# Performance work log

Measured on AMD Instinct MI355X. Metric: run time of the kernel, lower is better.

## Reference

```python
import jax, jax.numpy as jnp
import numpy as np

N = 50000       # num nodes
E_DIR = 250000  # directed edges; doubled with inverses -> 500000
R = 100         # num relations; doubled -> 200
D = 32          # input/hidden dim
L = 6           # num layers
B = 4           # batch of queries
K = 33          # 1 positive + 32 negative tails
EPS = 1e-6


def setup_inputs() -> dict:
    key = jax.random.key(0)
    ks = jax.random.split(key, 12)
    src = jax.random.randint(ks[0], (E_DIR,), 0, N)
    dst = jax.random.randint(ks[1], (E_DIR,), 0, N)
    rel = jax.random.randint(ks[2], (E_DIR,), 0, R)
    # graph.undirected(add_inverse=True): append (t, h, r + R)
    edge_list = jnp.concatenate([
        jnp.stack([src, dst, rel], -1),
        jnp.stack([dst, src, rel + R], -1)], 0).astype(jnp.int32)
    h0 = jax.random.randint(ks[3], (B, 1), 0, N)
    h_index = jnp.tile(h0, (1, K)).astype(jnp.int32)   # constant per row (asserted by module)
    t_index = jax.random.randint(ks[4], (B, K), 0, N).astype(jnp.int32)
    r0 = jax.random.randint(ks[5], (B, 1), 0, R)
    r_index = jnp.tile(r0, (1, K)).astype(jnp.int32)
    s = 0.1
    query_emb = jax.random.normal(ks[6], (2 * R, D)) * s
    rel_W = jax.random.normal(ks[7], (L, D, 2 * R * D)) * s          # relation_linear per layer
    rel_b = jax.random.normal(ks[8], (L, 2 * R * D)) * s
    lin_W = jax.random.normal(ks[9], (L, 13 * D, D)) / np.sqrt(13 * D)
    lin_b = jnp.zeros((L, D))
    F = 2 * D
    mlp_W1 = jax.random.normal(ks[10], (F, F)) / np.sqrt(F)
    mlp_b1 = jnp.zeros((F,))
    mlp_W2 = jax.random.normal(ks[11], (F, 1)) / np.sqrt(F)
    mlp_b2 = jnp.zeros((1,))
    return dict(edge_list=edge_list, h_index=h_index, t_index=t_index, r_index=r_index,
                query_emb=query_emb, rel_W=rel_W, rel_b=rel_b, lin_W=lin_W, lin_b=lin_b,
                mlp_W1=mlp_W1, mlp_b1=mlp_b1, mlp_W2=mlp_W2, mlp_b2=mlp_b2)


def _nbfnet(edge_list, h_index, t_index, r_index, query_emb, rel_W, rel_b,
            lin_W, lin_b, mlp_W1, mlp_b1, mlp_W2, mlp_b2):
    node_in, node_out, relation = edge_list[:, 0], edge_list[:, 1], edge_list[:, 2]
    E = node_in.shape[0]
    Bq = h_index.shape[0]
    dt = query_emb.dtype

    # negative_sample_to_tail (identity when rows of h_index are constant; kept faithful)
    is_t_neg = jnp.all(h_index == h_index[:, :1], axis=-1, keepdims=True)
    h_idx = jnp.where(is_t_neg, h_index, t_index)
    t_idx = jnp.where(is_t_neg, t_index, h_index)
    r_idx = jnp.where(is_t_neg, r_index, r_index + R)

    h0 = h_idx[:, 0]
    r0 = r_idx[:, 0]
    query = query_emb[r0]                                            # [B, D]
    # boundary scatter_add: boundary[h0[b], b] += query[b]
    boundary = jnp.zeros((N, Bq, D), dt).at[h0, jnp.arange(Bq)].add(query)

    arangeN = jnp.arange(N, dtype=node_out.dtype)
    out_all = jnp.concatenate([node_out, arangeN])                   # boundary acts as self-message
    edge_weight = jnp.ones((E,), dt)
    ew_all = jnp.concatenate([edge_weight, jnp.ones((N,), dt)])[:, None, None]
    cnt = jax.ops.segment_sum(jnp.ones((E + N,), dt), out_all, num_segments=N)  # msgs per node
    degree = jax.ops.segment_sum(edge_weight, node_out, num_segments=N) + 1.0
    scale = jnp.log(degree)
    scale = scale / scale.mean()
    scales = jnp.stack([jnp.ones_like(scale), scale, 1.0 / jnp.clip(scale, 1e-2)], -1)  # [N, 3]

    hidden = boundary
    for l in range(L):
        # dependent relation embeddings: [2R, B, D]
        rel_emb = (query @ rel_W[l] + rel_b[l]).reshape(Bq, 2 * R, D).transpose(1, 0, 2)
        msg = hidden[node_in] * rel_emb[relation]                    # distmult, [E, B, D]
        mraw = jnp.concatenate([msg, boundary], 0)                   # [E+N, B, D]
        m = mraw * ew_all
        cnt_b = cnt[:, None, None]
        mean = jax.ops.segment_sum(m, out_all, num_segments=N) / cnt_b
        sq_mean = jax.ops.segment_sum(mraw * mraw * ew_all, out_all, num_segments=N) / cnt_b
        mx = jax.ops.segment_max(m, out_all, num_segments=N)
        mn = jax.ops.segment_min(m, out_all, num_segments=N)
        std = jnp.sqrt(jnp.clip(sq_mean - mean * mean, EPS))
        feats = jnp.stack([mean, mx, mn, std], -1).reshape(N, Bq, 4 * D)
        update = (feats[..., None] * scales[:, None, None, :]).reshape(N, Bq, 12 * D)
        hidden = jax.nn.relu(jnp.concatenate([hidden, update], -1) @ lin_W[l] + lin_b[l])

    node_query = jnp.broadcast_to(query[None], (N, Bq, D))
    output = jnp.concatenate([hidden, node_query], -1)               # [N, B, 2D]
    feature = output.transpose(1, 0, 2)[jnp.arange(Bq)[:, None], t_idx]  # [B, K, 2D]
    hdd = jax.nn.relu(feature @ mlp_W1 + mlp_b1)
    score = (hdd @ mlp_W2 + mlp_b2)[..., 0]                          # [B, K]
    return score


def reference(edge_list, h_index, t_index, r_index, query_emb, rel_W, rel_b,
              lin_W, lin_b, mlp_W1, mlp_b1, mlp_W2, mlp_b2):
    return _nbfnet(edge_list, h_index, t_index, r_index, query_emb, rel_W, rel_b,
                   lin_W, lin_b, mlp_W1, mlp_b1, mlp_W2, mlp_b2)
```

## Files before the change

kernel.cpp:

```cpp
#include <hip/hip_runtime.h>
#include <hip/hip_bf16.h>

#define NN 50000
#define EE 500000
#define RR 100
#define DD 32
#define LL 6
#define BB 4
#define KK 33
#define BD 128
#define XDIM 416
#define NROWS (NN * BB)
#define FEPS 1e-6f
#define SCAN_B 1024
#define FB 16
#define FR 64
#define FSTR 132
#define RELSZ (2 * RR * BB * DD)

typedef __hip_bfloat16 bf16;
typedef unsigned short u16;

__device__ __forceinline__ float b2f(bf16 x) { return __bfloat162float(x); }
__device__ __forceinline__ float bfu2f(u16 u) { return __uint_as_float((unsigned)u << 16); }
__device__ __forceinline__ u16 f2bfu(float f) {
    unsigned u = __float_as_uint(f);
    return (u16)((u + 0x7FFFu + ((u >> 16) & 1u)) >> 16);
}
__device__ __forceinline__ float4 bf4(ushort4 u) {
    return make_float4(bfu2f(u.x), bfu2f(u.y), bfu2f(u.z), bfu2f(u.w));
}

__global__ void k_detect(const void* q, int* flag) {
    if (threadIdx.x == 0 && blockIdx.x == 0) {
        const unsigned short* u = (const unsigned short*)q;
        int wild = 0;
        for (int i = 0; i < 256; i++) {
            int expo = (u[i] >> 7) & 0xFF;
            if (expo >= 134) wild++;
        }
        *flag = (wild > 8) ? 1 : 0;
    }
}

__global__ void k_conv(const void* __restrict__ src, float* __restrict__ dst, int n,
                       const int* __restrict__ flag) {
    int i = blockIdx.x * 256 + threadIdx.x;
    if (i < n) {
        if (*flag) dst[i] = ((const float*)src)[i];
        else       dst[i] = b2f(((const bf16*)src)[i]);
    }
}

__global__ void k_degree(const int* __restrict__ el, int* __restrict__ cnt) {
    int e = blockIdx.x * blockDim.x + threadIdx.x;
    if (e < EE) atomicAdd(&cnt[el[e * 3 + 1]], 1);
}

__global__ void k_scan1(const int* __restrict__ cnt, int* __restrict__ incl, int* __restrict__ part) {
    __shared__ int sd[SCAN_B];
    int tid = threadIdx.x;
    int i = blockIdx.x * SCAN_B + tid;
    int v = (i < NN) ? cnt[i] : 0;
    sd[tid] = v;
    __syncthreads();
    for (int off = 1; off < SCAN_B; off <<= 1) {
        int t = (tid >= off) ? sd[tid - off] : 0;
        __syncthreads();
        sd[tid] += t;
        __syncthreads();
    }
    if (i < NN) incl[i] = sd[tid];
    if (tid == SCAN_B - 1) part[blockIdx.x] = sd[tid];
}

__global__ void k_scan2(int* part, int nb) {
    if (threadIdx.x == 0 && blockIdx.x == 0) {
        int run = 0;
        for (int i = 0; i < nb; i++) { int t = part[i]; part[i] = run; run += t; }
    }
}

__global__ void k_scan3(const int* __restrict__ incl, const int* __restrict__ part, int* __restrict__ row_ptr) {
    int i = blockIdx.x * blockDim.x + threadIdx.x;
    if (i < NN) row_ptr[i + 1] = incl[i] + part[i / SCAN_B];
    if (i == 0) row_ptr[0] = 0;
}

__global__ void k_scatter(const int* __restrict__ el, const int* __restrict__ row_ptr,
                          int* __restrict__ cur, int2* __restrict__ csr) {
    int e = blockIdx.x * blockDim.x + threadIdx.x;
    if (e < EE) {
        int dst = el[e * 3 + 1];
        int pos = row_ptr[dst] + atomicAdd(&cur[dst], 1);
        csr[pos] = make_int2(el[e * 3 + 0], el[e * 3 + 2]);
    }
}

__global__ void k_scale_sum(const int* __restrict__ cnt, float* __restrict__ ssum) {
    __shared__ float sd[256];
    int i = blockIdx.x * 256 + threadIdx.x;
    float v = (i < NN) ? logf((float)(cnt[i] + 1)) : 0.f;
    sd[threadIdx.x] = v;
    __syncthreads();
    for (int off = 128; off; off >>= 1) {
        if (threadIdx.x < off) sd[threadIdx.x] += sd[threadIdx.x + off];
        __syncthreads();
    }
    if (threadIdx.x == 0) atomicAdd(ssum, sd[0]);
}

__global__ void k_scale_fin(const int* __restrict__ cnt, const float* __restrict__ ssum,
                            float2* __restrict__ scales) {
    int i = blockIdx.x * 256 + threadIdx.x;
    if (i < NN) {
        float mean = *ssum / (float)NN;
        float s = logf((float)(cnt[i] + 1)) / mean;
        scales[i] = make_float2(s, 1.f / fmaxf(s, 0.01f));
    }
}

__global__ void k_prep(const int* __restrict__ h_index, const int* __restrict__ t_index,
                       const int* __restrict__ r_index, const float* __restrict__ query_emb,
                       int* __restrict__ h0, int* __restrict__ t_sel,
                       float* __restrict__ query) {
    __shared__ int s_h0[BB], s_r0[BB], s_neg[BB];
    int tid = threadIdx.x;
    if (tid < BB) {
        int h00 = h_index[tid * KK];
        int alleq = 1;
        for (int k = 1; k < KK; k++) alleq &= (h_index[tid * KK + k] == h00) ? 1 : 0;
        s_neg[tid] = alleq;
        s_h0[tid] = alleq ? h00 : t_index[tid * KK];
        s_r0[tid] = alleq ? r_index[tid * KK] : r_index[tid * KK] + RR;
        h0[tid] = s_h0[tid];
    }
    __syncthreads();
    for (int i = tid; i < BB * KK; i += blockDim.x) {
        int b = i / KK;
        t_sel[i] = s_neg[b] ? t_index[i] : h_index[i];
    }
    for (int i = tid; i < BB * DD; i += blockDim.x) {
        int b = i / DD, d = i - b * DD;
        query[i] = query_emb[s_r0[b] * DD + d];
    }
}

__global__ void k_rel_emb_all(const float* __restrict__ query, const float* __restrict__ relW,
                              const float* __restrict__ relb, float* __restrict__ rel_emb) {
    int gi = blockIdx.x * 256 + threadIdx.x;
    if (gi >= LL * RELSZ) return;
    int l = gi / RELSZ;
    int i = gi - l * RELSZ;
    int r = i / BD;
    int bd = i - r * BD;
    int b = bd >> 5, d = bd & 31;
    const float* relWl = relW + (size_t)l * DD * 2 * RR * DD;
    const float* relbl = relb + (size_t)l * 2 * RR * DD;
    float acc = relbl[r * DD + d];
    #pragma unroll 8
    for (int k = 0; k < DD; k++)
        acc += query[b * DD + k] * relWl[k * (2 * RR * DD) + r * DD + d];
    rel_emb[gi] = acc;
}

__global__ void k_reorg(const float* __restrict__ linWf, float* __restrict__ Wre) {
    int i = blockIdx.x * 256 + threadIdx.x;
    if (i >= LL * XDIM * DD) return;
    int l = i / (XDIM * DD);
    int rem = i - l * (XDIM * DD);
    int r = rem >> 5, c = rem & 31;
    int src;
    if (r < 384) {
        int k = r / 3, p = r - k * 3;
        int d = k & 31, s = k >> 5;
        src = 32 + d * 12 + s * 3 + p;
    } else {
        src = r - 384;
    }
    Wre[i] = linWf[(size_t)l * XDIM * DD + src * 32 + c];
}

#define EDGE_ACC(h4, r4)                                                          \
    {                                                                             \
        float v0 = h4.x * r4.x, v1 = h4.y * r4.y, v2 = h4.z * r4.z, v3 = h4.w * r4.w; \
        s0 += v0; s1 += v1; s2 += v2; s3 += v3;                                   \
        q0 += v0 * v0; q1 += v1 * v1; q2 += v2 * v2; q3 += v3 * v3;               \
        mx0 = fmaxf(mx0, v0); mx1 = fmaxf(mx1, v1); mx2 = fmaxf(mx2, v2); mx3 = fmaxf(mx3, v3); \
        mn0 = fminf(mn0, v0); mn1 = fminf(mn1, v1); mn2 = fminf(mn2, v2); mn3 = fminf(mn3, v3); \
    }

__global__ __launch_bounds__(512, 8) void k_fused(
    const int* __restrict__ row_ptr, const int2* __restrict__ csr,
    const float2* __restrict__ scales, const float* __restrict__ query,
    const int* __restrict__ h0v, const float* __restrict__ rel_emb,
    const u16* __restrict__ hin, u16* __restrict__ hout,
    const float* __restrict__ Wre, const float* __restrict__ lbl, int l0) {
    __shared__ float sx[FR * FSTR];
    int tid = threadIdx.x;
    int nb0 = blockIdx.x * FB;
    const float4 zf4 = make_float4(0.f, 0.f, 0.f, 0.f);

    {
        int ni = tid >> 5;
        int n = nb0 + ni;
        int t = tid & 31;
        int b = t >> 3;
        int dq = t & 7;
        int boff = b * DD + dq * 4;
        int h0b = h0v[b];
        float4 qv = *(const float4*)&query[boff];

        float4 bv = (h0b == n) ? qv : zf4;
        float s0 = bv.x, s1 = bv.y, s2 = bv.z, s3 = bv.w;
        float q0 = bv.x * bv.x, q1 = bv.y * bv.y, q2 = bv.z * bv.z, q3 = bv.w * bv.w;
        float mx0 = bv.x, mx1 = bv.y, mx2 = bv.z, mx3 = bv.w;
        float mn0 = bv.x, mn1 = bv.y, mn2 = bv.z, mn3 = bv.w;

        int e0 = row_ptr[n], e1 = row_ptr[n + 1];
        int e = e0;
        if (l0) {
            for (; e + 2 <= e1; e += 2) {
                int2 sa = csr[e];
                int2 sb = csr[e + 1];
                float4 ra = *(const float4*)&rel_emb[(size_t)sa.y * BD + boff];
                float4 rb = *(const float4*)&rel_emb[(size_t)sb.y * BD + boff];
                float4 ha = (sa.x == h0b) ? qv : zf4;
                float4 hb = (sb.x == h0b) ? qv : zf4;
                EDGE_ACC(ha, ra);
                EDGE_ACC(hb, rb);
            }
            if (e < e1) {
                int2 sr = csr[e];
                float4 r4 = *(const float4*)&rel_emb[(size_t)sr.y * BD + boff];
                float4 h4 = (sr.x == h0b) ? qv : zf4;
                EDGE_ACC(h4, r4);
            }
        } else {
            for (; e + 4 <= e1; e += 4) {
                int2 sa = csr[e];
                int2 sb = csr[e + 1];
                int2 sc2 = csr[e + 2];
                int2 sd2 = csr[e + 3];
                ushort4 hau = *(const ushort4*)&hin[(size_t)sa.x * BD + boff];
                float4 ra = *(const float4*)&rel_emb[(size_t)sa.y * BD + boff];
                ushort4 hbu = *(const ushort4*)&hin[(size_t)sb.x * BD + boff];
                float4 rb = *(const float4*)&rel_emb[(size_t)sb.y * BD + boff];
                ushort4 hcu = *(const ushort4*)&hin[(size_t)sc2.x * BD + boff];
                float4 rc = *(const float4*)&rel_emb[(size_t)sc2.y * BD + boff];
                ushort4 hdu = *(const ushort4*)&hin[(size_t)sd2.x * BD + boff];
                float4 rd = *(const float4*)&rel_emb[(size_t)sd2.y * BD + boff];
                float4 ha = bf4(hau), hb = bf4(hbu), hc = bf4(hcu), hd = bf4(hdu);
                EDGE_ACC(ha, ra);
                EDGE_ACC(hb, rb);
                EDGE_ACC(hc, rc);
                EDGE_ACC(hd, rd);
            }
            for (; e + 2 <= e1; e += 2) {
                int2 sa = csr[e];
                int2 sb = csr[e + 1];
                ushort4 hau = *(const ushort4*)&hin[(size_t)sa.x * BD + boff];
                float4 ra = *(const float4*)&rel_emb[(size_t)sa.y * BD + boff];
                ushort4 hbu = *(const ushort4*)&hin[(size_t)sb.x * BD + boff];
                float4 rb = *(const float4*)&rel_emb[(size_t)sb.y * BD + boff];
                float4 ha = bf4(hau), hb = bf4(hbu);
                EDGE_ACC(ha, ra);
                EDGE_ACC(hb, rb);
            }
            if (e < e1) {
                int2 sr = csr[e];
                ushort4 hu = *(const ushort4*)&hin[(size_t)sr.x * BD + boff];
                float4 r4 = *(const float4*)&rel_emb[(size_t)sr.y * BD + boff];
                float4 h4 = bf4(hu);
                EDGE_ACC(h4, r4);
            }
        }
        float cinv = 1.f / (float)(e1 - e0 + 1);
        float me0 = s0 * cinv, me1 = s1 * cinv, me2 = s2 * cinv, me3 = s3 * cinv;
        float sd0 = sqrtf(fmaxf(q0 * cinv - me0 * me0, FEPS));
        float sd1 = sqrtf(fmaxf(q1 * cinv - me1 * me1, FEPS));
        float sd2 = sqrtf(fmaxf(q2 * cinv - me2 * me2, FEPS));
        float sd3 = sqrtf(fmaxf(q3 * cinv - me3 * me3, FEPS));

        int d0 = dq * 4;
        float* dst = &sx[(ni * BB + b) * FSTR];
        *(float4*)&dst[0 * 32 + d0] = make_float4(me0, me1, me2, me3);
        *(float4*)&dst[1 * 32 + d0] = make_float4(mx0, mx1, mx2, mx3);
        *(float4*)&dst[2 * 32 + d0] = make_float4(mn0, mn1, mn2, mn3);
        *(float4*)&dst[3 * 32 + d0] = make_float4(sd0, sd1, sd2, sd3);
    }
    __syncthreads();

    int lr = tid & (FR - 1);
    int c0 = __builtin_amdgcn_readfirstlane((tid >> 6) << 2);
    int grow = blockIdx.x * FR + lr;
    float2 sc = scales[grow >> 2];
    const float* __restrict__ Wv = Wre;
    const float* __restrict__ Wh = Wre + 384 * 32;

    float a0[4], a1[4], a2[4];
    #pragma unroll
    for (int c = 0; c < 4; c++) { a0[c] = lbl[c0 + c]; a1[c] = 0.f; a2[c] = 0.f; }

    const float* xr = &sx[lr * FSTR];
    #pragma unroll 4
    for (int k = 0; k < 128; k++) {
        float x = xr[k];
        const float* w = &Wv[(size_t)k * 96 + c0];
        #pragma unroll
        for (int c = 0; c < 4; c++) {
            a0[c] = fmaf(x, w[c], a0[c]);
            a1[c] = fmaf(x, w[32 + c], a1[c]);
            a2[c] = fmaf(x, w[64 + c], a2[c]);
        }
    }
    if (l0) {
        int nB = grow >> 2, bB = grow & 3;
        bool selfq = (h0v[bB] == nB);
        const float* qrow = &query[bB * DD];
        #pragma unroll
        for (int q = 0; q < 8; q++) {
            float4 h4 = selfq ? *(const float4*)&qrow[q * 4] : zf4;
            float hx[4] = {h4.x, h4.y, h4.z, h4.w};
            #pragma unroll
            for (int j = 0; j < 4; j++) {
                const float* wh = &Wh[(size_t)(q * 4 + j) * 32 + c0];
                float x = hx[j];
                #pragma unroll
                for (int c = 0; c < 4; c++) a0[c] = fmaf(x, wh[c], a0[c]);
            }
        }
    } else {
        const unsigned* hrow32 = (const unsigned*)&hin[(size_t)grow * 32];
        #pragma unroll
        for (int q4 = 0; q4 < 4; q4++) {
            uint4 r4 = *(const uint4*)&hrow32[q4 * 4];
            unsigned uu[4] = {r4.x, r4.y, r4.z, r4.w};
            #pragma unroll
            for (int m = 0; m < 4; m++) {
                float xlo = __uint_as_float(uu[m] << 16);
                float xhi = __uint_as_float(uu[m] & 0xFFFF0000u);
                int kb = q4 * 8 + m * 2;
                const float* whl = &Wh[(size_t)kb * 32 + c0];
                const float* whh = &Wh[(size_t)(kb + 1) * 32 + c0];
                #pragma unroll
                for (int c = 0; c < 4; c++) a0[c] = fmaf(xlo, whl[c], a0[c]);
                #pragma unroll
                for (int c = 0; c < 4; c++) a0[c] = fmaf(xhi, whh[c], a0[c]);
            }
        }
    }

    float4 y;
    y.x = fmaxf(a0[0] + sc.x * a1[0] + sc.y * a2[0], 0.f);
    y.y = fmaxf(a0[1] + sc.x * a1[1] + sc.y * a2[1], 0.f);
    y.z = fmaxf(a0[2] + sc.x * a1[2] + sc.y * a2[2], 0.f);
    y.w = fmaxf(a0[3] + sc.x * a1[3] + sc.y * a2[3], 0.f);
    ushort4 yo;
    yo.x = f2bfu(y.x); yo.y = f2bfu(y.y); yo.z = f2bfu(y.z); yo.w = f2bfu(y.w);
    *(ushort4*)&hout[(size_t)grow * 32 + c0] = yo;
}

__global__ void k_score(const u16* __restrict__ hidden, const float* __restrict__ query,
                        const int* __restrict__ t_sel,
                        const float* __restrict__ W1, const float* __restrict__ b1,
                        const float* __restrict__ W2, const float* __restrict__ b2v,
                        void* __restrict__ out, const int* __restrict__ flag) {
    int bk = blockIdx.x;
    int b = bk / KK;
    int j = threadIdx.x;
    int t = t_sel[bk];
    __shared__ float feat[2 * DD];
    feat[j] = (j < DD) ? bfu2f(hidden[(size_t)t * BD + b * DD + j]) : query[b * DD + (j - DD)];
    __syncthreads();
    float acc = b1[j];
    #pragma unroll 8
    for (int i = 0; i < 2 * DD; i++) acc += feat[i] * W1[i * 2 * DD + j];
    float h = fmaxf(acc, 0.f);
    float c = h * W2[j];
    for (int off = 32; off; off >>= 1) c += __shfl_down(c, off);
    if (j == 0) {
        float r = c + b2v[0];
        if (*flag) ((float*)out)[bk] = r;
        else       ((bf16*)out)[bk] = __float2bfloat16(r);
    }
}

extern "C" void kernel_launch(void* const* d_in, const int* in_sizes, int n_in,
                              void* d_out, int out_size, void* d_ws, size_t ws_size,
                              hipStream_t stream) {
    const int* el = (const int*)d_in[0];
    const int* h_index = (const int*)d_in[1];
    const int* t_index = (const int*)d_in[2];
    const int* r_index = (const int*)d_in[3];

    char* ws = (char*)d_ws;
    size_t off = 0;
    auto alloc = [&](size_t bytes) -> void* {
        void* p = ws + off;
        off = (off + bytes + 255) & ~(size_t)255;
        return p;
    };
    int* row_ptr = (int*)alloc((NN + 1) * 4);
    int* cnt = (int*)alloc(NN * 4);
    int* cur = (int*)alloc(NN * 4);
    int* incl = (int*)alloc(NN * 4);
    int* part = (int*)alloc(64 * 4);
    int2* csr = (int2*)alloc((size_t)EE * 8);
    float2* scales = (float2*)alloc((size_t)NN * 8);
    float* query = (float*)alloc(BB * DD * 4);
    int* h0 = (int*)alloc(BB * 4);
    int* t_sel = (int*)alloc(BB * KK * 4);
    float* ssum = (float*)alloc(4);
    int* dflag = (int*)alloc(4);
    float* rel_emb = (float*)alloc((size_t)LL * RELSZ * 4);
    float* qe_f   = (float*)alloc((size_t)2 * RR * DD * 4);
    float* relW_f = (float*)alloc((size_t)LL * DD * 2 * RR * DD * 4);
    float* relb_f = (float*)alloc((size_t)LL * 2 * RR * DD * 4);
    float* linW_f = (float*)alloc((size_t)LL * XDIM * DD * 4);
    float* linb_f = (float*)alloc((size_t)LL * DD * 4);
    float* Wre    = (float*)alloc((size_t)LL * XDIM * DD * 4);
    float* w1_f   = (float*)alloc(4 * DD * DD * 4);
    float* b1_f   = (float*)alloc(2 * DD * 4);
    float* w2_f   = (float*)alloc(2 * DD * 4);
    float* b2_f   = (float*)alloc(4);
    u16* hid0 = (u16*)alloc((size_t)NN * BD * 2);
    u16* hid1 = (u16*)alloc((size_t)NN * BD * 2);

    hipMemsetAsync(cnt, 0, NN * 4, stream);
    hipMemsetAsync(cur, 0, NN * 4, stream);
    hipMemsetAsync(ssum, 0, 4, stream);

    k_detect<<<1, 64, 0, stream>>>(d_in[4], dflag);
    auto conv = [&](int idx, float* dst, int n) {
        k_conv<<<(n + 255) / 256, 256, 0, stream>>>(d_in[idx], dst, n, dflag);
    };
    conv(4, qe_f, 2 * RR * DD);
    conv(5, relW_f, LL * DD * 2 * RR * DD);
    conv(6, relb_f, LL * 2 * RR * DD);
    conv(7, linW_f, LL * XDIM * DD);
    conv(8, linb_f, LL * DD);
    conv(9, w1_f, 4 * DD * DD);
    conv(10, b1_f, 2 * DD);
    conv(11, w2_f, 2 * DD);
    conv(12, b2_f, 1);
    k_reorg<<<(LL * XDIM * DD + 255) / 256, 256, 0, stream>>>(linW_f, Wre);

    k_degree<<<(EE + 255) / 256, 256, 0, stream>>>(el, cnt);
    int nb = (NN + SCAN_B - 1) / SCAN_B;
    k_scan1<<<nb, SCAN_B, 0, stream>>>(cnt, incl, part);
    k_scan2<<<1, 64, 0, stream>>>(part, nb);
    k_scan3<<<(NN + 255) / 256, 256, 0, stream>>>(incl, part, row_ptr);
    k_scatter<<<(EE + 255) / 256, 256, 0, stream>>>(el, row_ptr, cur, csr);
    k_scale_sum<<<(NN + 255) / 256, 256, 0, stream>>>(cnt, ssum);
    k_scale_fin<<<(NN + 255) / 256, 256, 0, stream>>>(cnt, ssum, scales);
    k_prep<<<1, 128, 0, stream>>>(h_index, t_index, r_index, qe_f, h0, t_sel, query);
    k_rel_emb_all<<<(LL * RELSZ + 255) / 256, 256, 0, stream>>>(query, relW_f, relb_f, rel_emb);

    u16* hin = hid0;
    u16* hout = hid1;
    for (int l = 0; l < LL; l++) {
        k_fused<<<NN / FB, 512, 0, stream>>>(
            row_ptr, csr, scales, query, h0, rel_emb + (size_t)l * RELSZ, hin, hout,
            Wre + (size_t)l * XDIM * DD, linb_f + l * DD, (l == 0) ? 1 : 0);
        u16* tmp = hin; hin = hout; hout = tmp;
    }
    k_score<<<BB * KK, 2 * DD, 0, stream>>>(hin, query, t_sel, w1_f, b1_f, w2_f, b2_f,
                                            d_out, dflag);
}
```

Baseline: 700.4 us.

## Store relation embeddings in bf16 and split edges across half-warps

Relation embeddings are now stored as bf16 instead of fp32, halving their gather traffic. The edge aggregation is restructured so each thread handles 8 features with 16-byte loads, and the two half-warps process alternating edges, merged by xor-shuffles. This adds memory-level parallelism per node and cuts per-edge load count. The cost is bf16 rounding of the relation embeddings and extra shuffle work at the end.

```diff
diff --git a/kernel.cpp b/kernel.cpp
--- a/kernel.cpp
+++ b/kernel.cpp
@@ -1,5 +1,6 @@
 #include <hip/hip_runtime.h>
 #include <hip/hip_bf16.h>
+#include <math.h>
 
 #define NN 50000
 #define EE 500000
@@ -27,9 +28,6 @@
     unsigned u = __float_as_uint(f);
     return (u16)((u + 0x7FFFu + ((u >> 16) & 1u)) >> 16);
 }
-__device__ __forceinline__ float4 bf4(ushort4 u) {
-    return make_float4(bfu2f(u.x), bfu2f(u.y), bfu2f(u.z), bfu2f(u.w));
-}
 
 __global__ void k_detect(const void* q, int* flag) {
     if (threadIdx.x == 0 && blockIdx.x == 0) {
@@ -147,7 +145,7 @@
 }
 
 __global__ void k_rel_emb_all(const float* __restrict__ query, const float* __restrict__ relW,
-                              const float* __restrict__ relb, float* __restrict__ rel_emb) {
+                              const float* __restrict__ relb, u16* __restrict__ rel_emb) {
     int gi = blockIdx.x * 256 + threadIdx.x;
     if (gi >= LL * RELSZ) return;
     int l = gi / RELSZ;
@@ -161,7 +159,7 @@
     #pragma unroll 8
     for (int k = 0; k < DD; k++)
         acc += query[b * DD + k] * relWl[k * (2 * RR * DD) + r * DD + d];
-    rel_emb[gi] = acc;
+    rel_emb[gi] = f2bfu(acc);
 }
 
 __global__ void k_reorg(const float* __restrict__ linWf, float* __restrict__ Wre) {
@@ -181,19 +179,46 @@
     Wre[i] = linWf[(size_t)l * XDIM * DD + src * 32 + c];
 }
 
-#define EDGE_ACC(h4, r4)                                                          \
-    {                                                                             \
-        float v0 = h4.x * r4.x, v1 = h4.y * r4.y, v2 = h4.z * r4.z, v3 = h4.w * r4.w; \
-        s0 += v0; s1 += v1; s2 += v2; s3 += v3;                                   \
-        q0 += v0 * v0; q1 += v1 * v1; q2 += v2 * v2; q3 += v3 * v3;               \
-        mx0 = fmaxf(mx0, v0); mx1 = fmaxf(mx1, v1); mx2 = fmaxf(mx2, v2); mx3 = fmaxf(mx3, v3); \
-        mn0 = fminf(mn0, v0); mn1 = fminf(mn1, v1); mn2 = fminf(mn2, v2); mn3 = fminf(mn3, v3); \
+#define EDGE_ACC8(HU, RU)                                                       \
+    {                                                                           \
+        unsigned hw[4] = {HU.x, HU.y, HU.z, HU.w};                              \
+        unsigned rw[4] = {RU.x, RU.y, RU.z, RU.w};                              \
+        _Pragma("unroll")                                                       \
+        for (int m = 0; m < 4; m++) {                                           \
+            float hl = __uint_as_float(hw[m] << 16);                            \
+            float hh = __uint_as_float(hw[m] & 0xFFFF0000u);                    \
+            float rl = __uint_as_float(rw[m] << 16);                            \
+            float rh = __uint_as_float(rw[m] & 0xFFFF0000u);                    \
+            float v0 = hl * rl, v1 = hh * rh;                                   \
+            s[2 * m] += v0; s[2 * m + 1] += v1;                                 \
+            q[2 * m] = fmaf(v0, v0, q[2 * m]);                                  \
+            q[2 * m + 1] = fmaf(v1, v1, q[2 * m + 1]);                          \
+            mx[2 * m] = fmaxf(mx[2 * m], v0); mx[2 * m + 1] = fmaxf(mx[2 * m + 1], v1); \
+            mn[2 * m] = fminf(mn[2 * m], v0); mn[2 * m + 1] = fminf(mn[2 * m + 1], v1); \
+        }                                                                       \
+    }
+
+#define EDGE_ACC8_Q(SEL, RU)                                                    \
+    {                                                                           \
+        unsigned rw[4] = {RU.x, RU.y, RU.z, RU.w};                              \
+        _Pragma("unroll")                                                       \
+        for (int m = 0; m < 4; m++) {                                           \
+            float rl = __uint_as_float(rw[m] << 16);                            \
+            float rh = __uint_as_float(rw[m] & 0xFFFF0000u);                    \
+            float v0 = (SEL) ? qv[2 * m] * rl : 0.f;                            \
+            float v1 = (SEL) ? qv[2 * m + 1] * rh : 0.f;                        \
+            s[2 * m] += v0; s[2 * m + 1] += v1;                                 \
+            q[2 * m] = fmaf(v0, v0, q[2 * m]);                                  \
+            q[2 * m + 1] = fmaf(v1, v1, q[2 * m + 1]);                          \
+            mx[2 * m] = fmaxf(mx[2 * m], v0); mx[2 * m + 1] = fmaxf(mx[2 * m + 1], v1); \
+            mn[2 * m] = fminf(mn[2 * m], v0); mn[2 * m + 1] = fminf(mn[2 * m + 1], v1); \
+        }                                                                       \
     }
 
 __global__ __launch_bounds__(512, 8) void k_fused(
     const int* __restrict__ row_ptr, const int2* __restrict__ csr,
     const float2* __restrict__ scales, const float* __restrict__ query,
-    const int* __restrict__ h0v, const float* __restrict__ rel_emb,
+    const int* __restrict__ h0v, const u16* __restrict__ rel_emb,
     const u16* __restrict__ hin, u16* __restrict__ hout,
     const float* __restrict__ Wre, const float* __restrict__ lbl, int l0) {
     __shared__ float sx[FR * FSTR];
@@ -205,89 +230,92 @@
         int ni = tid >> 5;
         int n = nb0 + ni;
         int t = tid & 31;
-        int b = t >> 3;
-        int dq = t & 7;
-        int boff = b * DD + dq * 4;
+        int half = t >> 4;
+        int tt = t & 15;
+        int b = tt >> 2;
+        int d0 = (tt & 3) * 8;
+        int boff = b * DD + d0;
         int h0b = h0v[b];
-        float4 qv = *(const float4*)&query[boff];
-
-        float4 bv = (h0b == n) ? qv : zf4;
-        float s0 = bv.x, s1 = bv.y, s2 = bv.z, s3 = bv.w;
-        float q0 = bv.x * bv.x, q1 = bv.y * bv.y, q2 = bv.z * bv.z, q3 = bv.w * bv.w;
-        float mx0 = bv.x, mx1 = bv.y, mx2 = bv.z, mx3 = bv.w;
-        float mn0 = bv.x, mn1 = bv.y, mn2 = bv.z, mn3 = bv.w;
+
+        float qv[8];
+        *(float4*)&qv[0] = *(const float4*)&query[boff];
+        *(float4*)&qv[4] = *(const float4*)&query[boff + 4];
+
+        float s[8], q[8], mx[8], mn[8];
+        bool isq = (h0b == n);
+        #pragma unroll
+        for (int j = 0; j < 8; j++) {
+            if (half == 0) {
+                float bvj = isq ? qv[j] : 0.f;
+                s[j] = bvj; q[j] = bvj * bvj; mx[j] = bvj; mn[j] = bvj;
+            } else {
+                s[j] = 0.f; q[j] = 0.f; mx[j] = -INFINITY; mn[j] = INFINITY;
+            }
+        }
 
         int e0 = row_ptr[n], e1 = row_ptr[n + 1];
-        int e = e0;
+        int e = e0 + half;
         if (l0) {
-            for (; e + 2 <= e1; e += 2) {
+            for (; e + 2 < e1; e += 4) {
                 int2 sa = csr[e];
-                int2 sb = csr[e + 1];
-                float4 ra = *(const float4*)&rel_emb[(size_t)sa.y * BD + boff];
-                float4 rb = *(const float4*)&rel_emb[(size_t)sb.y * BD + boff];
-                float4 ha = (sa.x == h0b) ? qv : zf4;
-                float4 hb = (sb.x == h0b) ? qv : zf4;
-                EDGE_ACC(ha, ra);
-                EDGE_ACC(hb, rb);
+                int2 sb = csr[e + 2];
+                uint4 ra = *(const uint4*)&rel_emb[(size_t)sa.y * BD + boff];
+                uint4 rb = *(const uint4*)&rel_emb[(size_t)sb.y * BD + boff];
+                bool sela = (sa.x == h0b), selb = (sb.x == h0b);
+                EDGE_ACC8_Q(sela, ra);
+                EDGE_ACC8_Q(selb, rb);
             }
             if (e < e1) {
-                int2 sr = csr[e];
-                float4 r4 = *(const float4*)&rel_emb[(size_t)sr.y * BD + boff];
-                float4 h4 = (sr.x == h0b) ? qv : zf4;
-                EDGE_ACC(h4, r4);
+                int2 sa = csr[e];
+                uint4 ra = *(const uint4*)&rel_emb[(size_t)sa.y * BD + boff];
+                bool sela = (sa.x == h0b);
+                EDGE_ACC8_Q(sela, ra);
             }
         } else {
-            for (; e + 4 <= e1; e += 4) {
+            for (; e + 2 < e1; e += 4) {
                 int2 sa = csr[e];
-                int2 sb = csr[e + 1];
-                int2 sc2 = csr[e + 2];
-                int2 sd2 = csr[e + 3];
-                ushort4 hau = *(const ushort4*)&hin[(size_t)sa.x * BD + boff];
-                float4 ra = *(const float4*)&rel_emb[(size_t)sa.y * BD + boff];
-                ushort4 hbu = *(const ushort4*)&hin[(size_t)sb.x * BD + boff];
-                float4 rb = *(const float4*)&rel_emb[(size_t)sb.y * BD + boff];
-                ushort4 hcu = *(const ushort4*)&hin[(size_t)sc2.x * BD + boff];
-                float4 rc = *(const float4*)&rel_emb[(size_t)sc2.y * BD + boff];
-                ushort4 hdu = *(const ushort4*)&hin[(size_t)sd2.x * BD + boff];
-                float4 rd = *(const float4*)&rel_emb[(size_t)sd2.y * BD + boff];
-                float4 ha = bf4(hau), hb = bf4(hbu), hc = bf4(hcu), hd = bf4(hdu);
-                EDGE_ACC(ha, ra);
-                EDGE_ACC(hb, rb);
-                EDGE_ACC(hc, rc);
-                EDGE_ACC(hd, rd);
-            }
-            for (; e + 2 <= e1; e += 2) {
+                int2 sb = csr[e + 2];
+                uint4 ha = *(const uint4*)&hin[(size_t)sa.x * BD + boff];
+                uint4 ra = *(const uint4*)&rel_emb[(size_t)sa.y * BD + boff];
+                uint4 hb = *(const uint4*)&hin[(size_t)sb.x * BD + boff];
+                uint4 rb = *(const uint4*)&rel_emb[(size_t)sb.y * BD + boff];
+                EDGE_ACC8(ha, ra);
+                EDGE_ACC8(hb, rb);
+            }
+            if (e < e1) {
                 int2 sa = csr[e];
-                int2 sb = csr[e + 1];
-                ushort4 hau = *(const ushort4*)&hin[(size_t)sa.x * BD + boff];
-                float4 ra = *(const float4*)&rel_emb[(size_t)sa.y * BD + boff];
-                ushort4 hbu = *(const ushort4*)&hin[(size_t)sb.x * BD + boff];
-                float4 rb = *(const float4*)&rel_emb[(size_t)sb.y * BD + boff];
-                float4 ha = bf4(hau), hb = bf4(hbu);
-                EDGE_ACC(ha, ra);
-                EDGE_ACC(hb, rb);
-            }
-            if (e < e1) {
-                int2 sr = csr[e];
-                ushort4 hu = *(const ushort4*)&hin[(size_t)sr.x * BD + boff];
-                float4 r4 = *(const float4*)&rel_emb[(size_t)sr.y * BD + boff];
-                float4 h4 = bf4(hu);
-                EDGE_ACC(h4, r4);
-            }
-        }
-        float cinv = 1.f / (float)(e1 - e0 + 1);
-        float me0 = s0 * cinv, me1 = s1 * cinv, me2 = s2 * cinv, me3 = s3 * cinv;
-        float sd0 = sqrtf(fmaxf(q0 * cinv - me0 * me0, FEPS));
-        float sd1 = sqrtf(fmaxf(q1 * cinv - me1 * me1, FEPS));
-        float sd2 = sqrtf(fmaxf(q2 * cinv - me2 * me2, FEPS));
-        float sd3 = sqrtf(fmaxf(q3 * cinv - me3 * me3, FEPS));
-
-        int d0 = dq * 4;
-        float* dst = &sx[(ni * BB + b) * FSTR];
-        *(float4*)&dst[0 * 32 + d0] = make_float4(me0, me1, me2, me3);
-        *(float4*)&dst[1 * 32 + d0] = make_float4(mx0, mx1, mx2, mx3);
-        *(float4*)&dst[2 * 32 + d0] = make_float4(mn0, mn1, mn2, mn3);
-        *(float4*)&dst[3 * 32 + d0] = make_float4(sd0, sd1, sd2, sd3);
+                uint4 ha = *(const uint4*)&hin[(size_t)sa.x * BD + boff];
+                uint4 ra = *(const uint4*)&rel_emb[(size_t)sa.y * BD + boff];
+                EDGE_ACC8(ha, ra);
+            }
+        }
+
+        #pragma unroll
+        for (int j = 0; j < 8; j++) {
+            s[j] += __shfl_xor(s[j], 16);
+            q[j] += __shfl_xor(q[j], 16);
+            mx[j] = fmaxf(mx[j], __shfl_xor(mx[j], 16));
+            mn[j] = fminf(mn[j], __shfl_xor(mn[j], 16));
+        }
+
+        if (half == 0) {
+            float cinv = 1.f / (float)(e1 - e0 + 1);
+            float me[8], sd[8];
+            #pragma unroll
+            for (int j = 0; j < 8; j++) {
+                me[j] = s[j] * cinv;
+                sd[j] = sqrtf(fmaxf(q[j] * cinv - me[j] * me[j], FEPS));
+            }
+            float* dst = &sx[(ni * BB + b) * FSTR];
+            *(float4*)&dst[0 * 32 + d0]     = *(float4*)&me[0];
+            *(float4*)&dst[0 * 32 + d0 + 4] = *(float4*)&me[4];
+            *(float4*)&dst[1 * 32 + d0]     = *(float4*)&mx[0];
+            *(float4*)&dst[1 * 32 + d0 + 4] = *(float4*)&mx[4];
+            *(float4*)&dst[2 * 32 + d0]     = *(float4*)&mn[0];
+            *(float4*)&dst[2 * 32 + d0 + 4] = *(float4*)&mn[4];
+            *(float4*)&dst[3 * 32 + d0]     = *(float4*)&sd[0];
+            *(float4*)&dst[3 * 32 + d0 + 4] = *(float4*)&sd[4];
+        }
     }
     __syncthreads();
 
@@ -413,7 +441,7 @@
     int* t_sel = (int*)alloc(BB * KK * 4);
     float* ssum = (float*)alloc(4);
     int* dflag = (int*)alloc(4);
-    float* rel_emb = (float*)alloc((size_t)LL * RELSZ * 4);
+    u16* rel_emb = (u16*)alloc((size_t)LL * RELSZ * 2);
     float* qe_f   = (float*)alloc((size_t)2 * RR * DD * 4);
     float* relW_f = (float*)alloc((size_t)LL * DD * 2 * RR * DD * 4);
     float* relb_f = (float*)alloc((size_t)LL * 2 * RR * DD * 4);
```

Result: slower. 1.351 ms (+92.9%).
